# Optimization experiments

Measured on AMD Instinct MI355X. Metric: run time of the kernel, lower is better.

## Reference

```python
import jax, jax.numpy as jnp
import numpy as np

L, H, LATENT, DM, DH, FF = 4, 4, 256, 768, 192, 1024
EPS = 1e-6      # fast_transformers RecurrentLinearAttention eps
LN_EPS = 1e-5


def make_pe(d_model=LATENT, max_len=5000):
    pos = np.arange(max_len, dtype=np.float32)[:, None]
    div = np.exp(np.arange(0, d_model, 2, dtype=np.float32) * (-np.log(10000.0) / d_model))
    pe = np.zeros((max_len, d_model), np.float32)
    pe[:, 0::2] = np.sin(pos * div)
    pe[:, 1::2] = np.cos(pos * div)
    return jnp.asarray(pe)

PE = make_pe()


def layer_norm(x, g, b):
    m = x.mean(-1, keepdims=True)
    v = ((x - m) ** 2).mean(-1, keepdims=True)
    return (x - m) * jax.lax.rsqrt(v + LN_EPS) * g + b


def setup_inputs() -> dict:
    key = jax.random.key(0)
    ks = jax.random.split(key, 16)
    bs, nj, nf, T, A, C = 8, 25, 6, 80, 6, 12
    s = 0.02
    return dict(
        x=jax.random.normal(ks[0], (bs, nj, nf, T), jnp.float32),
        y=jax.random.randint(ks[1], (bs, A), 0, C),
        ind_map=jnp.sort(jax.random.randint(ks[2], (T, bs), 0, A), axis=0),
        act_tstamps=jnp.sort(jax.random.randint(ks[3], (bs, A), 1, T + 1), axis=1).at[:, -1].set(T),
        skel_W=jax.random.normal(ks[4], (nj * nf, LATENT), jnp.float32) * s,
        skel_b=jnp.zeros((LATENT,), jnp.float32),
        muQuery=jax.random.normal(ks[5], (C, LATENT), jnp.float32),
        sigmaQuery=jax.random.normal(ks[6], (C, LATENT), jnp.float32),
        Wq=jax.random.normal(ks[7], (L, DM, DM), jnp.float32) * s,
        bq=jnp.zeros((L, DM), jnp.float32),
        Wk=jax.random.normal(ks[8], (L, DM, DM), jnp.float32) * s,
        bk=jnp.zeros((L, DM), jnp.float32),
        Wv=jax.random.normal(ks[9], (L, DM, DM), jnp.float32) * s,
        bv=jnp.zeros((L, DM), jnp.float32),
        Wo=jax.random.normal(ks[10], (L, DM, DM), jnp.float32) * s,
        bo=jnp.zeros((L, DM), jnp.float32),
        W1=jax.random.normal(ks[11], (L, DM, FF), jnp.float32) * s,
        b1=jnp.zeros((L, FF), jnp.float32),
        W2=jax.random.normal(ks[12], (L, FF, DM), jnp.float32) * s,
        b2=jnp.zeros((L, DM), jnp.float32),
        ln1_g=jnp.ones((L, DM), jnp.float32), ln1_b=jnp.zeros((L, DM), jnp.float32),
        ln2_g=jnp.ones((L, DM), jnp.float32), ln2_b=jnp.zeros((L, DM), jnp.float32),
        lnf_g=jnp.ones((DM,), jnp.float32), lnf_b=jnp.zeros((DM,), jnp.float32),
    )


def _fwd(x, y, ind_map, act_tstamps, skel_W, skel_b, muQuery, sigmaQuery,
         Wq, bq, Wk, bk, Wv, bv, Wo, bo, W1, b1, W2, b2,
         ln1_g, ln1_b, ln2_g, ln2_b, lnf_g, lnf_b):
    bs, nj, nf, T = x.shape
    # skeleton embedding: [T, bs, njoints*nfeats] @ W -> [T, bs, LATENT]
    xe = x.transpose(3, 0, 1, 2).reshape(T, bs, nj * nf) @ skel_W + skel_b
    mu_q = muQuery[y]        # [bs, A, LATENT]
    sig_q = sigmaQuery[y]
    barange = jnp.arange(bs)

    @jax.checkpoint
    def step(carry, inputs):
        S, Z = carry                         # [L,bs,H,DH,DH], [L,bs,H,DH]
        t, xt, ind_t = inputs
        cm = mu_q[barange, ind_t]            # gather per-sample current action query
        cs = sig_q[barange, ind_t]
        xseq = jnp.stack([cm, cs, xt], 0)    # [3, bs, LATENT]
        start = jnp.where(t == 0, 0, t + 2)  # PositionalEncoding(last_pos=t, offset=2)
        pe3 = jax.lax.dynamic_slice_in_dim(PE, start, 3, 0)
        xseq = xseq + pe3[:, None, :]
        h = xseq.transpose(1, 0, 2).reshape(bs, 3 * LATENT)  # flatten -> [bs, DM]
        nS, nZ = [], []
        for l in range(L):
            q = (h @ Wq[l] + bq[l]).reshape(bs, H, DH)
            k = (h @ Wk[l] + bk[l]).reshape(bs, H, DH)
            v = (h @ Wv[l] + bv[l]).reshape(bs, H, DH)
            Q = jax.nn.elu(q) + 1.0          # linear-attention feature map
            K = jax.nn.elu(k) + 1.0
            Sl = S[l] + K[..., :, None] * v[..., None, :]   # state update S += k (x) v
            Zl = Z[l] + K
            inv = 1.0 / (jnp.einsum('bhd,bhd->bh', Q, Zl) + EPS)
            att = jnp.einsum('bhd,bhdm,bh->bhm', Q, Sl, inv).reshape(bs, DM)
            h1 = layer_norm(h + att @ Wo[l] + bo[l], ln1_g[l], ln1_b[l])
            ffn = jax.nn.relu(h1 @ W1[l] + b1[l]) @ W2[l] + b2[l]
            h = layer_norm(h1 + ffn, ln2_g[l], ln2_b[l])
            nS.append(Sl); nZ.append(Zl)
        h = layer_norm(h, lnf_g, lnf_b)      # encoder final norm
        return (jnp.stack(nS), jnp.stack(nZ)), h

    S0 = jnp.zeros((L, bs, H, DH, DH), x.dtype)
    Z0 = jnp.zeros((L, bs, H, DH), x.dtype)
    _, finals = jax.lax.scan(step, (S0, Z0), (jnp.arange(T), xe, ind_map))  # finals: [T,bs,DM]
    tsel = jnp.maximum(act_tstamps - 1, 0)                       # [bs, A]
    mu = finals[:, :, :LATENT][tsel, barange[:, None]]           # [bs, A, LATENT]
    logvar = finals[:, :, LATENT:2 * LATENT][tsel, barange[:, None]]
    return mu, logvar


def reference(x, y, ind_map, act_tstamps, skel_W, skel_b, muQuery, sigmaQuery,
              Wq, bq, Wk, bk, Wv, bv, Wo, bo, W1, b1, W2, b2,
              ln1_g, ln1_b, ln2_g, ln2_b, lnf_g, lnf_b):
    return _fwd(x, y, ind_map, act_tstamps, skel_W, skel_b, muQuery, sigmaQuery,
                Wq, bq, Wk, bk, Wv, bv, Wo, bo, W1, b1, W2, b2,
                ln1_g, ln1_b, ln2_g, ln2_b, lnf_g, lnf_b)
```

## Files before the change

kernel.cpp:

```cpp
#include <hip/hip_runtime.h>
#include <math.h>

#define TT 80
#define BS 8
#define NA 6
#define DMODEL 768
#define DH 192
#define FFD 1024
#define NROWS 640
#define NQKV 2304

typedef __bf16 bf16;
typedef __bf16 bf16x8 __attribute__((ext_vector_type(8)));
typedef float  f32x4  __attribute__((ext_vector_type(4)));

__device__ __forceinline__ void row_ms(const float* __restrict__ st, int row,
                                       float& m, float& rs) {
    float s1 = st[row * 2], s2 = st[row * 2 + 1];
    m = s1 * (1.0f / 768.0f);
    float var = s2 * (1.0f / 768.0f) - m * m;
    rs = rsqrtf(var + 1e-5f);
}

struct TJob { const float* src; bf16* dst; int ldsrc, Kd, n0, k0; };

__global__ __launch_bounds__(256) void prep_k(
        const float* __restrict__ x, const int* __restrict__ y,
        const int* __restrict__ ind_map,
        const float* __restrict__ skel_W, const float* __restrict__ skel_b,
        const float* __restrict__ muQ, const float* __restrict__ sigQ,
        const float* __restrict__ Wq, const float* __restrict__ Wk,
        const float* __restrict__ Wv, const float* __restrict__ Wo,
        const float* __restrict__ W1, const float* __restrict__ W2,
        bf16* __restrict__ qkvT, bf16* __restrict__ woT,
        bf16* __restrict__ w1T, bf16* __restrict__ w2T,
        float* __restrict__ h, bf16* __restrict__ h0B,
        float* __restrict__ stats) {
    __shared__ float tile[32][33];
    __shared__ float xrow[152];
    int bid = blockIdx.x, tid = threadIdx.x;
    if (bid < 15360) {
        TJob J;
        int l = bid / 3840, r = bid % 3840;
        if (r < 1728) {
            int kt = r % 24, nt = r / 24;
            J.k0 = kt * 32; J.n0 = nt * 32; J.Kd = 768; J.ldsrc = 768;
            J.dst = qkvT + (size_t)l * NQKV * DMODEL;
            if (J.n0 < 768)       { J.src = Wq + (size_t)l * 589824 + J.n0; }
            else if (J.n0 < 1536) { J.src = Wk + (size_t)l * 589824 + (J.n0 - 768); }
            else                  { J.src = Wv + (size_t)l * 589824 + (J.n0 - 1536); }
        } else if (r < 2304) {
            int r2 = r - 1728; int kt = r2 % 24, nt = r2 / 24;
            J.k0 = kt * 32; J.n0 = nt * 32; J.Kd = 768; J.ldsrc = 768;
            J.src = Wo + (size_t)l * 589824 + J.n0;
            J.dst = woT + (size_t)l * 589824;
        } else if (r < 3072) {
            int r2 = r - 2304; int kt = r2 % 24, nt = r2 / 24;
            J.k0 = kt * 32; J.n0 = nt * 32; J.Kd = 768; J.ldsrc = 1024;
            J.src = W1 + (size_t)l * 786432 + J.n0;
            J.dst = w1T + (size_t)l * 786432;
        } else {
            int r2 = r - 3072; int kt = r2 % 32, nt = r2 / 32;
            J.k0 = kt * 32; J.n0 = nt * 32; J.Kd = 1024; J.ldsrc = 768;
            J.src = W2 + (size_t)l * 786432 + J.n0;
            J.dst = w2T + (size_t)l * 786432;
        }
        int tx = tid & 31, ty = tid >> 5;
#pragma unroll
        for (int i = 0; i < 4; i++) {
            int rr = ty + 8 * i;
            tile[rr][tx] = J.src[(size_t)(J.k0 + rr) * J.ldsrc + tx];
        }
        __syncthreads();
#pragma unroll
        for (int i = 0; i < 4; i++) {
            int rr = ty + 8 * i;
            J.dst[(size_t)(J.n0 + rr) * J.Kd + J.k0 + tx] = (bf16)tile[tx][rr];
        }
    } else {
        int r = bid - 15360;
        int t = r >> 3, b = r & 7;
        int c = tid;
        if (c < 16) {
            int arr = c >> 3, l = (c >> 1) & 3, j = c & 1;
            stats[arr * 5120 + l * 1280 + r * 2 + j] = 0.0f;
        }
        if (c < 150) xrow[c] = x[(b * 150 + c) * TT + t];
        __syncthreads();
        float acc = skel_b[c];
        for (int jf = 0; jf < 150; jf++) acc += xrow[jf] * skel_W[jf * 256 + c];
        int ind_t = ind_map[t * 8 + b];
        int yb = y[b * NA + ind_t];
        float cm = muQ[yb * 256 + c];
        float cs = sigQ[yb * 256 + c];
        int start = (t == 0) ? 0 : (t + 2);
        float div = expf((float)(c & ~1) * (-9.210340371976184f / 256.0f));
        float p0, p1, p2;
        if (c & 1) {
            p0 = cosf((float)start * div);
            p1 = cosf((float)(start + 1) * div);
            p2 = cosf((float)(start + 2) * div);
        } else {
            p0 = sinf((float)start * div);
            p1 = sinf((float)(start + 1) * div);
            p2 = sinf((float)(start + 2) * div);
        }
        float* hr = h + (size_t)r * DMODEL;
        float v0 = cm + p0, v1 = cs + p1, v2 = acc + p2;
        hr[c] = v0; hr[c + 256] = v1; hr[c + 512] = v2;
        bf16* hb = h0B + (size_t)r * DMODEL;
        hb[c] = (bf16)v0; hb[c + 256] = (bf16)v1; hb[c + 512] = (bf16)v2;
    }
}

template <int EPI, int ANORM, int RNORM>
__global__ __launch_bounds__(256) void gemm_mfma(
        const bf16* __restrict__ Ab, const float* __restrict__ Af,
        const float* __restrict__ stA, const float* __restrict__ gA,
        const float* __restrict__ bA,
        const bf16* __restrict__ Bt,
        const float* __restrict__ bias_q, const float* __restrict__ bias_k,
        const float* __restrict__ bias_v,
        const float* __restrict__ residF, const float* __restrict__ stR,
        const float* __restrict__ gR, const float* __restrict__ bR,
        float* __restrict__ outF, bf16* __restrict__ outB,
        float* __restrict__ stOut, int N, int K) {
    __shared__ __attribute__((aligned(16))) bf16 As0[64][40];
    __shared__ __attribute__((aligned(16))) bf16 As1[64][40];
    __shared__ __attribute__((aligned(16))) bf16 Bs0[64][40];
    __shared__ __attribute__((aligned(16))) bf16 Bs1[64][40];
    int tid = threadIdx.x;
    int m0 = blockIdx.y * 64, n0 = blockIdx.x * 64;
    int w = tid >> 6, l = tid & 63;
    int lm = l & 15, lq = l >> 4;
    int sr = tid >> 2;
    int sk = (tid & 3) * 8;
    int arow = m0 + sr;
    const bf16* Brow = &Bt[(size_t)(n0 + sr) * K];
    f32x4 acc[4] = {};
    const bf16* Abrow = nullptr; const float* Afrow = nullptr;
    float mA = 0.f, rsA = 0.f;
    if (ANORM) {
        Afrow = &Af[(size_t)arow * K];
        row_ms(stA, arow, mA, rsA);
    } else {
        Abrow = &Ab[(size_t)arow * K];
    }
    uint4 a0, a1;
    f32x4 ax0a, ax0b, ax1a, ax1b;
    if (ANORM) {
        ax0a = *(const f32x4*)&Afrow[sk];      ax0b = *(const f32x4*)&Afrow[sk + 4];
        ax1a = *(const f32x4*)&Afrow[32 + sk]; ax1b = *(const f32x4*)&Afrow[36 + sk];
    } else {
        a0 = *(const uint4*)&Abrow[sk];
        a1 = *(const uint4*)&Abrow[32 + sk];
    }
    uint4 b0 = *(const uint4*)&Brow[sk];
    uint4 b1 = *(const uint4*)&Brow[32 + sk];
    for (int k0 = 0; k0 < K; k0 += 64) {
        __syncthreads();
        if (ANORM) {
            union { bf16 t[8]; uint4 u; } c0, c1;
            const float* gp = gA + k0 + sk;
            const float* bp = bA + k0 + sk;
#pragma unroll
            for (int j = 0; j < 4; j++) {
                c0.t[j]     = (bf16)((ax0a[j] - mA) * rsA * gp[j]      + bp[j]);
                c0.t[j + 4] = (bf16)((ax0b[j] - mA) * rsA * gp[j + 4]  + bp[j + 4]);
                c1.t[j]     = (bf16)((ax1a[j] - mA) * rsA * gp[32 + j] + bp[32 + j]);
                c1.t[j + 4] = (bf16)((ax1b[j] - mA) * rsA * gp[36 + j] + bp[36 + j]);
            }
            *(uint4*)&As0[sr][sk] = c0.u;
            *(uint4*)&As1[sr][sk] = c1.u;
        } else {
            *(uint4*)&As0[sr][sk] = a0;
            *(uint4*)&As1[sr][sk] = a1;
        }
        *(uint4*)&Bs0[sr][sk] = b0;
        *(uint4*)&Bs1[sr][sk] = b1;
        __syncthreads();
        int k2 = k0 + 64; if (k2 >= K) k2 = 0;
        if (ANORM) {
            ax0a = *(const f32x4*)&Afrow[k2 + sk];      ax0b = *(const f32x4*)&Afrow[k2 + sk + 4];
            ax1a = *(const f32x4*)&Afrow[k2 + 32 + sk]; ax1b = *(const f32x4*)&Afrow[k2 + 36 + sk];
        } else {
            a0 = *(const uint4*)&Abrow[k2 + sk];
            a1 = *(const uint4*)&Abrow[k2 + 32 + sk];
        }
        b0 = *(const uint4*)&Brow[k2 + sk];
        b1 = *(const uint4*)&Brow[k2 + 32 + sk];
        bf16x8 af0 = *(bf16x8*)&As0[w * 16 + lm][lq * 8];
        bf16x8 af1 = *(bf16x8*)&As1[w * 16 + lm][lq * 8];
#pragma unroll
        for (int nb = 0; nb < 4; nb++) {
            bf16x8 bfr = *(bf16x8*)&Bs0[nb * 16 + lm][lq * 8];
            acc[nb] = __builtin_amdgcn_mfma_f32_16x16x32_bf16(af0, bfr, acc[nb], 0, 0, 0);
        }
#pragma unroll
        for (int nb = 0; nb < 4; nb++) {
            bf16x8 bfr = *(bf16x8*)&Bs1[nb * 16 + lm][lq * 8];
            acc[nb] = __builtin_amdgcn_mfma_f32_16x16x32_bf16(af1, bfr, acc[nb], 0, 0, 0);
        }
    }
    if (EPI == 1) {
        float mR4[4], rsR4[4];
        if (RNORM) {
#pragma unroll
            for (int r = 0; r < 4; r++)
                row_ms(stR, m0 + w * 16 + lq * 4 + r, mR4[r], rsR4[r]);
        }
        float s1[4] = {0.f, 0.f, 0.f, 0.f}, s2[4] = {0.f, 0.f, 0.f, 0.f};
#pragma unroll
        for (int nb = 0; nb < 4; nb++) {
            int col = n0 + nb * 16 + lm;
            float bia = bias_q[col];
            float gc = 0.f, bc = 0.f;
            if (RNORM) { gc = gR[col]; bc = bR[col]; }
#pragma unroll
            for (int r = 0; r < 4; r++) {
                int row = m0 + w * 16 + lq * 4 + r;
                float rv = residF[(size_t)row * N + col];
                if (RNORM) rv = (rv - mR4[r]) * rsR4[r] * gc + bc;
                float v = acc[nb][r] + bia + rv;
                outF[(size_t)row * N + col] = v;
                s1[r] += v; s2[r] += v * v;
            }
        }
#pragma unroll
        for (int mk = 1; mk < 16; mk <<= 1) {
#pragma unroll
            for (int r = 0; r < 4; r++) {
                s1[r] += __shfl_xor(s1[r], mk, 64);
                s2[r] += __shfl_xor(s2[r], mk, 64);
            }
        }
        if (lm == 0) {
#pragma unroll
            for (int r = 0; r < 4; r++) {
                int row = m0 + w * 16 + lq * 4 + r;
                atomicAdd(&stOut[row * 2],     s1[r]);
                atomicAdd(&stOut[row * 2 + 1], s2[r]);
            }
        }
    } else {
#pragma unroll
        for (int nb = 0; nb < 4; nb++) {
            int col = n0 + nb * 16 + lm;
            float bia; bool do_elu = false;
            if (EPI == 0) {
                if (col < 768)       { bia = bias_q[col];        do_elu = true; }
                else if (col < 1536) { bia = bias_k[col - 768];  do_elu = true; }
                else                 { bia = bias_v[col - 1536]; }
            } else {
                bia = bias_q[col];
            }
#pragma unroll
            for (int r = 0; r < 4; r++) {
                int row = m0 + w * 16 + lq * 4 + r;
                float v = acc[nb][r] + bia;
                if (EPI == 0) {
                    if (do_elu) v = (v > 0.0f) ? (v + 1.0f) : expf(v);
                    outB[(size_t)row * N + col] = (bf16)v;
                } else {
                    outB[(size_t)row * N + col] = (bf16)fmaxf(v, 0.0f);
                }
            }
        }
    }
}

__global__ __launch_bounds__(320) void attn_k(
        const bf16* __restrict__ qkvB, bf16* __restrict__ att) {
    __shared__ __attribute__((aligned(16))) char smem[64000];
    bf16* Qs = (bf16*)smem;
    bf16* Ks = (bf16*)(smem + 32000);
    bf16* Aij = (bf16*)smem;
    bf16* VT = (bf16*)(smem + 16640);
    int bh = blockIdx.x / 3, part = blockIdx.x % 3;
    int bb = bh >> 2, hd = bh & 3;
    int tid = threadIdx.x;
    int w = tid >> 6, l = tid & 63;
    int lm = l & 15, lq = l >> 4;

    uint4 vreg[6];
#pragma unroll
    for (int u = 0; u < 6; u++) {
        int c = tid + 320 * u;
        int t = c / 24, cc = c % 24;
        int d0 = cc * 8;
        size_t g = (size_t)(t * 8 + bb) * NQKV + hd * DH + d0;
        uint4 qv = *(const uint4*)&qkvB[g];
        uint4 kv = *(const uint4*)&qkvB[g + 768];
        vreg[u]  = *(const uint4*)&qkvB[g + 1536];
        *(uint4*)&Qs[t * 200 + d0] = qv;
        *(uint4*)&Ks[t * 200 + d0] = kv;
    }
    __syncthreads();

    f32x4 acc[5] = {};
#pragma unroll
    for (int k0 = 0; k0 < 192; k0 += 32) {
        bf16x8 af = *(bf16x8*)&Qs[(w * 16 + lm) * 200 + lq * 8 + k0];
#pragma unroll
        for (int nb = 0; nb < 5; nb++) {
            bf16x8 bfr = *(bf16x8*)&Ks[(nb * 16 + lm) * 200 + lq * 8 + k0];
            acc[nb] = __builtin_amdgcn_mfma_f32_16x16x32_bf16(af, bfr, acc[nb], 0, 0, 0);
        }
    }
    float mval[5][4];
    float rs[4] = {0.f, 0.f, 0.f, 0.f};
#pragma unroll
    for (int nb = 0; nb < 5; nb++)
#pragma unroll
        for (int r = 0; r < 4; r++) {
            int t = w * 16 + lq * 4 + r, tau = nb * 16 + lm;
            float v = (tau <= t) ? acc[nb][r] : 0.0f;
            mval[nb][r] = v;
            rs[r] += v;
        }
#pragma unroll
    for (int mk = 1; mk < 16; mk <<= 1)
#pragma unroll
        for (int r = 0; r < 4; r++) rs[r] += __shfl_xor(rs[r], mk, 64);
    float inv[4];
#pragma unroll
    for (int r = 0; r < 4; r++) inv[r] = 1.0f / (rs[r] + 1e-6f);

    __syncthreads();

#pragma unroll
    for (int nb = 0; nb < 5; nb++)
#pragma unroll
        for (int r = 0; r < 4; r++)
            Aij[(w * 16 + lq * 4 + r) * 104 + nb * 16 + lm] = (bf16)mval[nb][r];
    *(uint2*)&Aij[(tid >> 2) * 104 + 80 + (tid & 3) * 4] = make_uint2(0u, 0u);
#pragma unroll
    for (int u = 0; u < 6; u++) {
        int c = tid + 320 * u;
        int t = c / 24, cc = c % 24;
        int d0 = cc * 8;
        bf16 tmp8[8];
        *(uint4*)tmp8 = vreg[u];
#pragma unroll
        for (int j = 0; j < 8; j++) VT[(d0 + j) * 104 + t] = tmp8[j];
    }
    if (tid < 192) {
        *(uint4*)&VT[tid * 104 + 80] = make_uint4(0u, 0u, 0u, 0u);
        *(uint4*)&VT[tid * 104 + 88] = make_uint4(0u, 0u, 0u, 0u);
    }
    __syncthreads();

#pragma unroll 1
    for (int nc = part * 4; nc < part * 4 + 4; nc++) {
        f32x4 a2 = {};
#pragma unroll
        for (int k0 = 0; k0 < 96; k0 += 32) {
            bf16x8 af = *(bf16x8*)&Aij[(w * 16 + lm) * 104 + lq * 8 + k0];
            bf16x8 bfr = *(bf16x8*)&VT[(nc * 16 + lm) * 104 + lq * 8 + k0];
            a2 = __builtin_amdgcn_mfma_f32_16x16x32_bf16(af, bfr, a2, 0, 0, 0);
        }
#pragma unroll
        for (int r = 0; r < 4; r++) {
            int t = w * 16 + lq * 4 + r;
            att[(size_t)(t * 8 + bb) * DMODEL + hd * DH + nc * 16 + lm] =
                (bf16)(a2[r] * inv[r]);
        }
    }
}

__device__ __forceinline__ float block_reduce_sum256(float v, float* sm4) {
#pragma unroll
    for (int off = 32; off > 0; off >>= 1) v += __shfl_down(v, off, 64);
    int lane = threadIdx.x & 63, wid = threadIdx.x >> 6;
    if (lane == 0) sm4[wid] = v;
    __syncthreads();
    float r = sm4[0] + sm4[1] + sm4[2] + sm4[3];
    __syncthreads();
    return r;
}

__global__ __launch_bounds__(256) void final_k(
        const float* __restrict__ tmp2, const float* __restrict__ st2,
        const float* __restrict__ g2, const float* __restrict__ b2,
        const int* __restrict__ act_ts,
        const float* __restrict__ gf, const float* __restrict__ bf_,
        float* __restrict__ out) {
    __shared__ float sm4[4];
    int ba = blockIdx.x;
    int b = ba / NA;
    int ts = act_ts[ba];
    int t = ts - 1; if (t < 0) t = 0;
    int row = t * 8 + b;
    const float* xr = tmp2 + (size_t)row * DMODEL;
    int c = threadIdx.x;
    float m2, rs2;
    row_ms(st2, row, m2, rs2);
    float x0 = (xr[c]       - m2) * rs2 * g2[c]       + b2[c];
    float x1 = (xr[c + 256] - m2) * rs2 * g2[c + 256] + b2[c + 256];
    float x2 = (xr[c + 512] - m2) * rs2 * g2[c + 512] + b2[c + 512];
    float m = block_reduce_sum256(x0 + x1 + x2, sm4) * (1.0f / 768.0f);
    float d0 = x0 - m, d1 = x1 - m, d2 = x2 - m;
    float v = block_reduce_sum256(d0 * d0 + d1 * d1 + d2 * d2, sm4) * (1.0f / 768.0f);
    float r = rsqrtf(v + 1e-5f);
    out[ba * 256 + c]            = d0 * r * gf[c] + bf_[c];
    out[48 * 256 + ba * 256 + c] = d1 * r * gf[c + 256] + bf_[c + 256];
}

extern "C" void kernel_launch(void* const* d_in, const int* in_sizes, int n_in,
                              void* d_out, int out_size, void* d_ws, size_t ws_size,
                              hipStream_t stream) {
    const float* x       = (const float*)d_in[0];
    const int*   y       = (const int*)d_in[1];
    const int*   ind_map = (const int*)d_in[2];
    const int*   act_ts  = (const int*)d_in[3];
    const float* skel_W  = (const float*)d_in[4];
    const float* skel_b  = (const float*)d_in[5];
    const float* muQ     = (const float*)d_in[6];
    const float* sigQ    = (const float*)d_in[7];
    const float* Wq = (const float*)d_in[8];   const float* bq = (const float*)d_in[9];
    const float* Wk = (const float*)d_in[10];  const float* bk = (const float*)d_in[11];
    const float* Wv = (const float*)d_in[12];  const float* bv = (const float*)d_in[13];
    const float* Wo = (const float*)d_in[14];  const float* bo = (const float*)d_in[15];
    const float* W1 = (const float*)d_in[16];  const float* b1 = (const float*)d_in[17];
    const float* W2 = (const float*)d_in[18];  const float* b2 = (const float*)d_in[19];
    const float* ln1_g = (const float*)d_in[20]; const float* ln1_b = (const float*)d_in[21];
    const float* ln2_g = (const float*)d_in[22]; const float* ln2_b = (const float*)d_in[23];
    const float* lnf_g = (const float*)d_in[24]; const float* lnf_b = (const float*)d_in[25];
    float* out = (float*)d_out;

    char* p = (char*)d_ws;
    const size_t R = (size_t)NROWS * DMODEL;
    float* h     = (float*)p; p += R * 4;
    float* tmp1  = (float*)p; p += R * 4;
    float* tmp2  = (float*)p; p += R * 4;
    float* stats = (float*)p; p += 10240 * 4;
    bf16* h0B    = (bf16*)p;  p += R * 2;
    bf16* qkvB   = (bf16*)p;  p += (size_t)NROWS * NQKV * 2;
    bf16* attB   = (bf16*)p;  p += R * 2;
    bf16* ffn1B  = (bf16*)p;  p += (size_t)NROWS * FFD * 2;
    bf16* qkvT   = (bf16*)p;  p += (size_t)4 * NQKV * DMODEL * 2;
    bf16* woT    = (bf16*)p;  p += (size_t)4 * DMODEL * DMODEL * 2;
    bf16* w1T    = (bf16*)p;  p += (size_t)4 * FFD * DMODEL * 2;
    bf16* w2T    = (bf16*)p;  p += (size_t)4 * DMODEL * FFD * 2;

    prep_k<<<16000, 256, 0, stream>>>(x, y, ind_map, skel_W, skel_b, muQ, sigQ,
                                      Wq, Wk, Wv, Wo, W1, W2,
                                      qkvT, woT, w1T, w2T, h, h0B, stats);

    dim3 gQKV(NQKV / 64, 10);
    dim3 g768(12, 10);
    dim3 g1024(16, 10);
    for (int l = 0; l < 4; l++) {
        const bf16* qkvTl = qkvT + (size_t)l * NQKV * DMODEL;
        const bf16* woTl  = woT  + (size_t)l * DMODEL * DMODEL;
        const bf16* w1Tl  = w1T  + (size_t)l * FFD * DMODEL;
        const bf16* w2Tl  = w2T  + (size_t)l * DMODEL * FFD;
        float* st1 = stats + l * 1280;
        float* st2 = stats + 5120 + l * 1280;
        const float* st2p = stats + 5120 + (l - 1) * 1280;
        const float* g2p = ln2_g + (l - 1) * DMODEL;
        const float* b2p = ln2_b + (l - 1) * DMODEL;

        if (l == 0)
            gemm_mfma<0, 0, 0><<<gQKV, 256, 0, stream>>>(
                h0B, nullptr, nullptr, nullptr, nullptr, qkvTl,
                bq, bk, bv,
                nullptr, nullptr, nullptr, nullptr,
                nullptr, qkvB, nullptr, NQKV, DMODEL);
        else
            gemm_mfma<0, 1, 0><<<gQKV, 256, 0, stream>>>(
                nullptr, tmp2, st2p, g2p, b2p, qkvTl,
                bq + l * DMODEL, bk + l * DMODEL, bv + l * DMODEL,
                nullptr, nullptr, nullptr, nullptr,
                nullptr, qkvB, nullptr, NQKV, DMODEL);

        attn_k<<<96, 320, 0, stream>>>(qkvB, attB);

        if (l == 0)
            gemm_mfma<1, 0, 0><<<g768, 256, 0, stream>>>(
                attB, nullptr, nullptr, nullptr, nullptr, woTl,
                bo, nullptr, nullptr,
                h, nullptr, nullptr, nullptr,
                tmp1, nullptr, st1, DMODEL, DMODEL);
        else
            gemm_mfma<1, 0, 1><<<g768, 256, 0, stream>>>(
                attB, nullptr, nullptr, nullptr, nullptr, woTl,
                bo + l * DMODEL, nullptr, nullptr,
                tmp2, st2p, g2p, b2p,
                tmp1, nullptr, st1, DMODEL, DMODEL);

        gemm_mfma<2, 1, 0><<<g1024, 256, 0, stream>>>(
            nullptr, tmp1, st1, ln1_g + l * DMODEL, ln1_b + l * DMODEL, w1Tl,
            b1 + l * FFD, nullptr, nullptr,
            nullptr, nullptr, nullptr, nullptr,
            nullptr, ffn1B, nullptr, FFD, DMODEL);

        gemm_mfma<1, 0, 1><<<g768, 256, 0, stream>>>(
            ffn1B, nullptr, nullptr, nullptr, nullptr, w2Tl,
            b2 + l * DMODEL, nullptr, nullptr,
            tmp1, st1, ln1_g + l * DMODEL, ln1_b + l * DMODEL,
            tmp2, nullptr, st2, DMODEL, FFD);
    }

    final_k<<<48, 256, 0, stream>>>(tmp2, stats + 5120 + 3 * 1280,
                                    ln2_g + 3 * DMODEL, ln2_b + 3 * DMODEL,
                                    act_ts, lnf_g, lnf_b, out);
}
```

Before: 441.2 us.

## Shrink GEMM tiles to 32x32 and feed normalized GEMMs from bf16 activations

Changes the MFMA GEMM from 64x64 tiles with 256 threads to 32x32 tiles with 128 threads, giving each launch about four times as many blocks. With only 120–360 blocks before, many of the GPU's compute units sat idle, and this spreads the work across them. The residual-add epilogues now also write a bf16 copy of their output. The layernorm-fused GEMMs read that bf16 copy instead of the fp32 tensor, which halves A-operand traffic but normalizes already-rounded values. Smaller tiles give less data reuse per block and more redundant B-operand loads.

```diff
diff --git a/kernel.cpp b/kernel.cpp
--- a/kernel.cpp
+++ b/kernel.cpp
@@ -20,6 +20,19 @@
     m = s1 * (1.0f / 768.0f);
     float var = s2 * (1.0f / 768.0f) - m * m;
     rs = rsqrtf(var + 1e-5f);
+}
+
+__device__ __forceinline__ uint4 norm8(uint4 raw, float m, float rs,
+                                       const float* __restrict__ gp,
+                                       const float* __restrict__ bp) {
+    union { bf16 t[8]; uint4 u; } in, out;
+    in.u = raw;
+#pragma unroll
+    for (int j = 0; j < 8; j++) {
+        float a = (float)in.t[j];
+        out.t[j] = (bf16)((a - m) * rs * gp[j] + bp[j]);
+    }
+    return out.u;
 }
 
 struct TJob { const float* src; bf16* dst; int ldsrc, Kd, n0, k0; };
@@ -114,8 +127,8 @@
 }
 
 template <int EPI, int ANORM, int RNORM>
-__global__ __launch_bounds__(256) void gemm_mfma(
-        const bf16* __restrict__ Ab, const float* __restrict__ Af,
+__global__ __launch_bounds__(128) void gemm_mfma(
+        const bf16* __restrict__ Ab,
         const float* __restrict__ stA, const float* __restrict__ gA,
         const float* __restrict__ bA,
         const bf16* __restrict__ Bt,
@@ -125,53 +138,31 @@
         const float* __restrict__ gR, const float* __restrict__ bR,
         float* __restrict__ outF, bf16* __restrict__ outB,
         float* __restrict__ stOut, int N, int K) {
-    __shared__ __attribute__((aligned(16))) bf16 As0[64][40];
-    __shared__ __attribute__((aligned(16))) bf16 As1[64][40];
-    __shared__ __attribute__((aligned(16))) bf16 Bs0[64][40];
-    __shared__ __attribute__((aligned(16))) bf16 Bs1[64][40];
+    __shared__ __attribute__((aligned(16))) bf16 As0[32][40];
+    __shared__ __attribute__((aligned(16))) bf16 As1[32][40];
+    __shared__ __attribute__((aligned(16))) bf16 Bs0[32][40];
+    __shared__ __attribute__((aligned(16))) bf16 Bs1[32][40];
     int tid = threadIdx.x;
-    int m0 = blockIdx.y * 64, n0 = blockIdx.x * 64;
+    int m0 = blockIdx.y * 32, n0 = blockIdx.x * 32;
     int w = tid >> 6, l = tid & 63;
     int lm = l & 15, lq = l >> 4;
     int sr = tid >> 2;
     int sk = (tid & 3) * 8;
     int arow = m0 + sr;
+    const bf16* Arow = &Ab[(size_t)arow * K];
     const bf16* Brow = &Bt[(size_t)(n0 + sr) * K];
-    f32x4 acc[4] = {};
-    const bf16* Abrow = nullptr; const float* Afrow = nullptr;
+    f32x4 acc[2] = {};
     float mA = 0.f, rsA = 0.f;
-    if (ANORM) {
-        Afrow = &Af[(size_t)arow * K];
-        row_ms(stA, arow, mA, rsA);
-    } else {
-        Abrow = &Ab[(size_t)arow * K];
-    }
-    uint4 a0, a1;
-    f32x4 ax0a, ax0b, ax1a, ax1b;
-    if (ANORM) {
-        ax0a = *(const f32x4*)&Afrow[sk];      ax0b = *(const f32x4*)&Afrow[sk + 4];
-        ax1a = *(const f32x4*)&Afrow[32 + sk]; ax1b = *(const f32x4*)&Afrow[36 + sk];
-    } else {
-        a0 = *(const uint4*)&Abrow[sk];
-        a1 = *(const uint4*)&Abrow[32 + sk];
-    }
+    if (ANORM) row_ms(stA, arow, mA, rsA);
+    uint4 a0 = *(const uint4*)&Arow[sk];
+    uint4 a1 = *(const uint4*)&Arow[32 + sk];
     uint4 b0 = *(const uint4*)&Brow[sk];
     uint4 b1 = *(const uint4*)&Brow[32 + sk];
     for (int k0 = 0; k0 < K; k0 += 64) {
         __syncthreads();
         if (ANORM) {
-            union { bf16 t[8]; uint4 u; } c0, c1;
-            const float* gp = gA + k0 + sk;
-            const float* bp = bA + k0 + sk;
-#pragma unroll
-            for (int j = 0; j < 4; j++) {
-                c0.t[j]     = (bf16)((ax0a[j] - mA) * rsA * gp[j]      + bp[j]);
-                c0.t[j + 4] = (bf16)((ax0b[j] - mA) * rsA * gp[j + 4]  + bp[j + 4]);
-                c1.t[j]     = (bf16)((ax1a[j] - mA) * rsA * gp[32 + j] + bp[32 + j]);
-                c1.t[j + 4] = (bf16)((ax1b[j] - mA) * rsA * gp[36 + j] + bp[36 + j]);
-            }
-            *(uint4*)&As0[sr][sk] = c0.u;
-            *(uint4*)&As1[sr][sk] = c1.u;
+            *(uint4*)&As0[sr][sk] = norm8(a0, mA, rsA, gA + k0 + sk, bA + k0 + sk);
+            *(uint4*)&As1[sr][sk] = norm8(a1, mA, rsA, gA + k0 + 32 + sk, bA + k0 + 32 + sk);
         } else {
             *(uint4*)&As0[sr][sk] = a0;
             *(uint4*)&As1[sr][sk] = a1;
@@ -180,24 +171,19 @@
         *(uint4*)&Bs1[sr][sk] = b1;
         __syncthreads();
         int k2 = k0 + 64; if (k2 >= K) k2 = 0;
-        if (ANORM) {
-            ax0a = *(const f32x4*)&Afrow[k2 + sk];      ax0b = *(const f32x4*)&Afrow[k2 + sk + 4];
-            ax1a = *(const f32x4*)&Afrow[k2 + 32 + sk]; ax1b = *(const f32x4*)&Afrow[k2 + 36 + sk];
-        } else {
-            a0 = *(const uint4*)&Abrow[k2 + sk];
-            a1 = *(const uint4*)&Abrow[k2 + 32 + sk];
-        }
+        a0 = *(const uint4*)&Arow[k2 + sk];
+        a1 = *(const uint4*)&Arow[k2 + 32 + sk];
         b0 = *(const uint4*)&Brow[k2 + sk];
         b1 = *(const uint4*)&Brow[k2 + 32 + sk];
         bf16x8 af0 = *(bf16x8*)&As0[w * 16 + lm][lq * 8];
         bf16x8 af1 = *(bf16x8*)&As1[w * 16 + lm][lq * 8];
 #pragma unroll
-        for (int nb = 0; nb < 4; nb++) {
+        for (int nb = 0; nb < 2; nb++) {
             bf16x8 bfr = *(bf16x8*)&Bs0[nb * 16 + lm][lq * 8];
             acc[nb] = __builtin_amdgcn_mfma_f32_16x16x32_bf16(af0, bfr, acc[nb], 0, 0, 0);
         }
 #pragma unroll
-        for (int nb = 0; nb < 4; nb++) {
+        for (int nb = 0; nb < 2; nb++) {
             bf16x8 bfr = *(bf16x8*)&Bs1[nb * 16 + lm][lq * 8];
             acc[nb] = __builtin_amdgcn_mfma_f32_16x16x32_bf16(af1, bfr, acc[nb], 0, 0, 0);
         }
@@ -211,7 +197,7 @@
         }
         float s1[4] = {0.f, 0.f, 0.f, 0.f}, s2[4] = {0.f, 0.f, 0.f, 0.f};
 #pragma unroll
-        for (int nb = 0; nb < 4; nb++) {
+        for (int nb = 0; nb < 2; nb++) {
             int col = n0 + nb * 16 + lm;
             float bia = bias_q[col];
             float gc = 0.f, bc = 0.f;
@@ -223,6 +209,7 @@
                 if (RNORM) rv = (rv - mR4[r]) * rsR4[r] * gc + bc;
                 float v = acc[nb][r] + bia + rv;
                 outF[(size_t)row * N + col] = v;
+                outB[(size_t)row * N + col] = (bf16)v;
                 s1[r] += v; s2[r] += v * v;
             }
         }
@@ -244,7 +231,7 @@
         }
     } else {
 #pragma unroll
-        for (int nb = 0; nb < 4; nb++) {
+        for (int nb = 0; nb < 2; nb++) {
             int col = n0 + nb * 16 + lm;
             float bia; bool do_elu = false;
             if (EPI == 0) {
@@ -435,6 +422,8 @@
     float* tmp2  = (float*)p; p += R * 4;
     float* stats = (float*)p; p += 10240 * 4;
     bf16* h0B    = (bf16*)p;  p += R * 2;
+    bf16* tmp1B  = (bf16*)p;  p += R * 2;
+    bf16* tmp2B  = (bf16*)p;  p += R * 2;
     bf16* qkvB   = (bf16*)p;  p += (size_t)NROWS * NQKV * 2;
     bf16* attB   = (bf16*)p;  p += R * 2;
     bf16* ffn1B  = (bf16*)p;  p += (size_t)NROWS * FFD * 2;
@@ -447,9 +436,9 @@
                                       Wq, Wk, Wv, Wo, W1, W2,
                                       qkvT, woT, w1T, w2T, h, h0B, stats);
 
-    dim3 gQKV(NQKV / 64, 10);
-    dim3 g768(12, 10);
-    dim3 g1024(16, 10);
+    dim3 gQKV(NQKV / 32, 20);
+    dim3 g768(24, 20);
+    dim3 g1024(32, 20);
     for (int l = 0; l < 4; l++) {
         const bf16* qkvTl = qkvT + (size_t)l * NQKV * DMODEL;
         const bf16* woTl  = woT  + (size_t)l * DMODEL * DMODEL;
@@ -462,14 +451,14 @@
         const float* b2p = ln2_b + (l - 1) * DMODEL;
 
         if (l == 0)
-            gemm_mfma<0, 0, 0><<<gQKV, 256, 0, stream>>>(
-                h0B, nullptr, nullptr, nullptr, nullptr, qkvTl,
+            gemm_mfma<0, 0, 0><<<gQKV, 128, 0, stream>>>(
+                h0B, nullptr, nullptr, nullptr, qkvTl,
                 bq, bk, bv,
                 nullptr, nullptr, nullptr, nullptr,
                 nullptr, qkvB, nullptr, NQKV, DMODEL);
         else
-            gemm_mfma<0, 1, 0><<<gQKV, 256, 0, stream>>>(
-                nullptr, tmp2, st2p, g2p, b2p, qkvTl,
+            gemm_mfma<0, 1, 0><<<gQKV, 128, 0, stream>>>(
+                tmp2B, st2p, g2p, b2p, qkvTl,
                 bq + l * DMODEL, bk + l * DMODEL, bv + l * DMODEL,
                 nullptr, nullptr, nullptr, nullptr,
                 nullptr, qkvB, nullptr, NQKV, DMODEL);
@@ -477,29 +466,29 @@
         attn_k<<<96, 320, 0, stream>>>(qkvB, attB);
 
         if (l == 0)
-            gemm_mfma<1, 0, 0><<<g768, 256, 0, stream>>>(
-                attB, nullptr, nullptr, nullptr, nullptr, woTl,
+            gemm_mfma<1, 0, 0><<<g768, 128, 0, stream>>>(
+                attB, nullptr, nullptr, nullptr, woTl,
                 bo, nullptr, nullptr,
                 h, nullptr, nullptr, nullptr,
-                tmp1, nullptr, st1, DMODEL, DMODEL);
+                tmp1, tmp1B, st1, DMODEL, DMODEL);
         else
-            gemm_mfma<1, 0, 1><<<g768, 256, 0, stream>>>(
-                attB, nullptr, nullptr, nullptr, nullptr, woTl,
+            gemm_mfma<1, 0, 1><<<g768, 128, 0, stream>>>(
+                attB, nullptr, nullptr, nullptr, woTl,
                 bo + l * DMODEL, nullptr, nullptr,
                 tmp2, st2p, g2p, b2p,
-                tmp1, nullptr, st1, DMODEL, DMODEL);
-
-        gemm_mfma<2, 1, 0><<<g1024, 256, 0, stream>>>(
-            nullptr, tmp1, st1, ln1_g + l * DMODEL, ln1_b + l * DMODEL, w1Tl,
+                tmp1, tmp1B, st1, DMODEL, DMODEL);
+
+        gemm_mfma<2, 1, 0><<<g1024, 128, 0, stream>>>(
+            tmp1B, st1, ln1_g + l * DMODEL, ln1_b + l * DMODEL, w1Tl,
             b1 + l * FFD, nullptr, nullptr,
             nullptr, nullptr, nullptr, nullptr,
             nullptr, ffn1B, nullptr, FFD, DMODEL);
 
-        gemm_mfma<1, 0, 1><<<g768, 256, 0, stream>>>(
-            ffn1B, nullptr, nullptr, nullptr, nullptr, w2Tl,
+        gemm_mfma<1, 0, 1><<<g768, 128, 0, stream>>>(
+            ffn1B, nullptr, nullptr, nullptr, w2Tl,
             b2 + l * DMODEL, nullptr, nullptr,
             tmp1, st1, ln1_g + l * DMODEL, ln1_b + l * DMODEL,
-            tmp2, nullptr, st2, DMODEL, FFD);
+            tmp2, tmp2B, st2, DMODEL, FFD);
     }
 
     final_k<<<48, 256, 0, stream>>>(tmp2, stats + 5120 + 3 * 1280,
```

After: 457.5 us. +3.7%, slower.
